# Performance work log

Hardware: AMD Instinct MI355X
Metric: run time of the kernel (lower is better)

The kernel has to match this reference:

```python
import jax, jax.numpy as jnp
import numpy as np

# BoeNet deterministic (greedy) BFS rollout reference.
# Assumptions (source truncated): GrowthPolicyNet ~ Linear(H,1)+sigmoid applied to
# node hidden + DEPTH_EMBED_SCALE * depth_embedding; greedy path expands when
# prob > greedy_threshold. Tree is materialized as a complete binary tree up to
# max_depth with per-node active masks (jit-friendly; honors data-dependent growth
# via masking instead of dynamic shapes). Pooling: mean over active nodes.

V, E, H = 32000, 512, 512
MAX_DEPTH = 3
DEPTH_EMBED_SCALE = 0.01
GREEDY_THRESHOLD = 0.5
PROB_MIN, PROB_MAX = 1e-7, 1.0 - 1e-7
EPS = 1e-8
SIB_SCALE = 1.0 / np.sqrt(H)


def setup_inputs() -> dict:
    key = jax.random.key(0)
    ks = jax.random.split(key, 8)
    B, S = 8, 512
    return {
        "tokens": jax.random.randint(ks[0], (B, S), 0, V),
        "emb": jax.random.normal(ks[1], (V, E), jnp.float32) * 0.02,
        "Wp": jax.random.normal(ks[2], (E, H), jnp.float32) / np.sqrt(E),
        "bp": jnp.zeros((H,), jnp.float32),
        "Wc": jax.random.normal(ks[3], (H, 2 * H), jnp.float32) / np.sqrt(H),
        "bc": jnp.zeros((2 * H,), jnp.float32),
        "Wg": jax.random.normal(ks[4], (H, 1), jnp.float32) / np.sqrt(H),
        "bg": jnp.zeros((1,), jnp.float32),
        "dep": jax.random.normal(ks[5], (MAX_DEPTH + 1, H), jnp.float32) * 0.01,
        "sib": jax.random.normal(ks[6], (2, H), jnp.float32) * 0.02,
        "Wout": jax.random.normal(ks[7], (H, V), jnp.float32) / np.sqrt(H),
        "bout": jnp.zeros((V,), jnp.float32),
    }


def reference(tokens, emb, Wp, bp, Wc, bc, Wg, bg, dep, sib, Wout, bout):
    B, S = tokens.shape
    N = B * S
    # h0: embedding lookup + projection, flattened to positions [N, H]
    h0 = (emb[tokens.reshape(N)] @ Wp + bp)  # [N, H]

    nodes = h0[:, None, :]                    # [N, 1, H] level-0 nodes
    active = jnp.ones((N, 1), h0.dtype)
    agg_sum = h0                              # root always counted
    agg_count = jnp.ones((N,), h0.dtype)

    for d in range(MAX_DEPTH):
        n = nodes.shape[1]
        # growth policy: sigmoid gate on node hidden + scaled depth embedding
        gate_in = nodes + DEPTH_EMBED_SCALE * dep[d]
        prob = jax.nn.sigmoid(jnp.einsum('nkh,ho->nko', gate_in, Wg)[..., 0] + bg[0])
        prob = jnp.clip(prob, PROB_MIN, PROB_MAX)           # [N, n]
        expand = (prob > GREEDY_THRESHOLD).astype(h0.dtype) * active  # [N, n]
        # children: Linear(H, 2H) split into left/right, plus sibling embeddings
        ch = (jnp.einsum('nkh,hj->nkj', nodes, Wc) + bc).reshape(N, 2 * n, H)
        sib_idx = jnp.tile(jnp.arange(2), n)                # [0,1,0,1,...]
        ch = ch + SIB_SCALE * sib[sib_idx]
        ch_active = jnp.repeat(expand, 2, axis=1)           # [N, 2n]
        agg_sum = agg_sum + jnp.einsum('nkh,nk->nh', ch, ch_active)
        agg_count = agg_count + ch_active.sum(axis=1)
        nodes, active = ch, ch_active

    pooled = agg_sum / jnp.maximum(agg_count, EPS)[:, None]  # mean pooling
    logits = pooled @ Wout + bout                            # [N, V]
    return logits.reshape(B, S, V)
```

## Files before the change

### kernel.cpp

```cpp
#include <hip/hip_runtime.h>
#include <cstdint>

#define BM 128
#define BN 128
#define BK 32

typedef __attribute__((ext_vector_type(8))) short short8;
typedef _Float16 half8 __attribute__((ext_vector_type(8)));
typedef __attribute__((ext_vector_type(4))) float floatx4;

union H8 { short8 s; half8 h; };

static constexpr float SIBS   = 0.044194173824159216f;
static constexpr float LS_INV = 1.0f / 2048.0f;

__device__ __forceinline__ unsigned short f2bf(float x){
    union { float f; unsigned u32; } v; v.f = x;
    unsigned r = ((v.u32 >> 16) & 1u) + 0x7fffu;
    return (unsigned short)((v.u32 + r) >> 16);
}
__device__ __forceinline__ void split_f16(float x, unsigned short& h, unsigned short& s){
    _Float16 hh = (_Float16)x;
    _Float16 ss = (_Float16)((x - (float)hh) * 2048.0f);
    union { _Float16 f; unsigned short u; } a, b;
    a.f = hh; b.f = ss;
    h = a.u; s = b.u;
}

#define GLDS(g, l) __builtin_amdgcn_global_load_lds( \
    (const __attribute__((address_space(1))) void*)(g), \
    (__attribute__((address_space(3))) void*)(l), 16, 0, 0)

__global__ void prep_split16_T(const float* __restrict__ src,
                               unsigned short* __restrict__ hiT,
                               unsigned short* __restrict__ lsT,
                               int R, int C)
{
    __shared__ float t[32][33];
    int c0 = blockIdx.x * 32, r0 = blockIdx.y * 32;
    int tx = threadIdx.x & 31, ty = threadIdx.x >> 5;
#pragma unroll
    for (int k = 0; k < 4; k++){
        int r = ty + k*8;
        t[r][tx] = src[(size_t)(r0 + r) * C + c0 + tx];
    }
    __syncthreads();
#pragma unroll
    for (int k = 0; k < 4; k++){
        int r = ty + k*8;
        float x = t[tx][r];
        unsigned short h, s;
        split_f16(x, h, s);
        size_t o = (size_t)(c0 + r) * R + r0 + tx;
        hiT[o] = h; lsT[o] = s;
    }
}

__global__ void prep_bf16_T(const float* __restrict__ src,
                            unsigned short* __restrict__ dstT,
                            int R, int C)
{
    __shared__ float t[32][33];
    int c0 = blockIdx.x * 32, r0 = blockIdx.y * 32;
    int tx = threadIdx.x & 31, ty = threadIdx.x >> 5;
#pragma unroll
    for (int k = 0; k < 4; k++){
        int r = ty + k*8;
        t[r][tx] = src[(size_t)(r0 + r) * C + c0 + tx];
    }
    __syncthreads();
#pragma unroll
    for (int k = 0; k < 4; k++){
        int r = ty + k*8;
        dstT[(size_t)(c0 + r) * R + r0 + tx] = f2bf(t[tx][r]);
    }
}

template<int MODE, int DEPTH>
__global__ __launch_bounds__(256, 2)
void gemm_k(const unsigned short* __restrict__ Abf,
            const float* __restrict__ Af32,
            const unsigned short* __restrict__ BTh,
            const unsigned short* __restrict__ BTl,
            const float* __restrict__ bias,
            const int* __restrict__ tokens,
            const float* __restrict__ emb,
            const float* __restrict__ sib,
            const unsigned char* __restrict__ eflag,
            float* __restrict__ nodes_next,
            float* __restrict__ agg,
            float* __restrict__ f32out,
            float* __restrict__ out,
            int N)
{
    constexpr int K = 512;
    __shared__ __align__(16) unsigned short Ah[BM*BK];
    __shared__ __align__(16) unsigned short Al[BM*BK];
    __shared__ __align__(16) unsigned short Bh[BK*BN];
    __shared__ __align__(16) unsigned short Bl[BK*BN];

    const int tid = threadIdx.x;
    const int w = tid >> 6, l = tid & 63;
    const int wr = w >> 1, wc = w & 1;
    const int row0 = blockIdx.x * BM;
    const int n0   = blockIdx.y * BN;
    const int q = l >> 4, lm = l & 15;

    floatx4 acc[4][4]  = {};
    floatx4 accx[4][4] = {};

    const float* aptr = nullptr;
    const int am = tid & 127, kq0 = tid >> 7;
    if (MODE == 0)      aptr = emb  + (long)tokens[row0 + am] * K;
    else if (MODE == 1) aptr = Af32 + (long)(row0 + am) * K;

    long arow0 = 0, arow1 = 0;
    if (MODE == 2){
        arow0 = (long)(row0 + l) * K;
        arow1 = (long)(row0 + 64 + l) * K;
    }
    const long brow0 = (long)(n0 + l) * K;
    const long brow1 = (long)(n0 + 64 + l) * K;

    for (int k0 = 0; k0 < K; k0 += BK){
        __syncthreads();
        GLDS(BTh + brow0 + k0 + w*8, (char*)Bh + w*2048);
        GLDS(BTh + brow1 + k0 + w*8, (char*)Bh + w*2048 + 1024);
        if (MODE <= 1){
            GLDS(BTl + brow0 + k0 + w*8, (char*)Bl + w*2048);
            GLDS(BTl + brow1 + k0 + w*8, (char*)Bl + w*2048 + 1024);
#pragma unroll
            for (int t = 0; t < 2; t++){
                int kq = kq0 + 2*t;
                const float* src = aptr + k0 + kq*8;
                float xs[8];
                *(floatx4*)&xs[0] = *(const floatx4*)(src);
                *(floatx4*)&xs[4] = *(const floatx4*)(src + 4);
                unsigned short h8[8], l8[8];
#pragma unroll
                for (int e = 0; e < 8; e++) split_f16(xs[e], h8[e], l8[e]);
                int s = kq*128 + am;
                *(short8*)&Ah[s*8] = *(const short8*)h8;
                *(short8*)&Al[s*8] = *(const short8*)l8;
            }
        } else {
            GLDS(Abf + arow0 + k0 + w*8, (char*)Ah + w*2048);
            GLDS(Abf + arow1 + k0 + w*8, (char*)Ah + w*2048 + 1024);
        }
        __syncthreads();

        H8 bh[4], bl[4];
#pragma unroll
        for (int j = 0; j < 4; j++){
            bh[j].s = *(const short8*)&Bh[(q*128 + wc*64 + j*16 + lm)*8];
            if (MODE <= 1)
                bl[j].s = *(const short8*)&Bl[(q*128 + wc*64 + j*16 + lm)*8];
        }
#pragma unroll
        for (int i = 0; i < 4; i++){
            H8 ah; ah.s = *(const short8*)&Ah[(q*128 + wr*64 + i*16 + lm)*8];
            if (MODE <= 1){
                H8 al; al.s = *(const short8*)&Al[(q*128 + wr*64 + i*16 + lm)*8];
#pragma unroll
                for (int j = 0; j < 4; j++)
                    acc[i][j]  = __builtin_amdgcn_mfma_f32_16x16x32_f16(ah.h, bh[j].h, acc[i][j], 0, 0, 0);
#pragma unroll
                for (int j = 0; j < 4; j++)
                    accx[i][j] = __builtin_amdgcn_mfma_f32_16x16x32_f16(ah.h, bl[j].h, accx[i][j], 0, 0, 0);
#pragma unroll
                for (int j = 0; j < 4; j++)
                    accx[i][j] = __builtin_amdgcn_mfma_f32_16x16x32_f16(al.h, bh[j].h, accx[i][j], 0, 0, 0);
            } else {
#pragma unroll
                for (int j = 0; j < 4; j++)
                    acc[i][j] = __builtin_amdgcn_mfma_f32_16x16x32_bf16(ah.s, bh[j].s, acc[i][j], 0, 0, 0);
            }
        }
    }

#pragma unroll
    for (int i = 0; i < 4; i++){
        int rbase = row0 + wr*64 + i*16 + q*4;
        unsigned char fl[4];
        if (MODE == 1){
#pragma unroll
            for (int r = 0; r < 4; r++) fl[r] = eflag[rbase + r];
        }
#pragma unroll
        for (int j = 0; j < 4; j++){
            int col = n0 + wc*64 + j*16 + lm;
            float badd = bias[col];
            int half = 0, h = 0;
            if (MODE == 1){
                half = col >> 9; h = col & 511;
                badd += SIBS * sib[half*512 + h];
            }
#pragma unroll
            for (int r = 0; r < 4; r++){
                int row = rbase + r;
                float v = acc[i][j][r];
                if (MODE <= 1) v += accx[i][j][r] * LS_INV;
                v += badd;
                if (MODE == 0){
                    f32out[(long)row*512 + col] = v;
                    agg[(long)row*512 + col]    = v;
                } else if (MODE == 1){
                    if (DEPTH < 2)
                        nodes_next[((long)(2*row + half))*512 + h] = v;
                    if (fl[r])
                        atomicAdd(&agg[((long)(row >> DEPTH))*512 + h], v);
                } else {
                    out[(long)row*(long)N + col] = v;
                }
            }
        }
    }
}

__global__ void gate_k(const float* __restrict__ nodes,
                       const float* __restrict__ Wg,
                       const float* __restrict__ bg,
                       const float* __restrict__ deprow,
                       const unsigned char* __restrict__ eprev,
                       unsigned char* __restrict__ e,
                       int depth)
{
    int row = blockIdx.x * 4 + (threadIdx.x >> 6);
    int l = threadIdx.x & 63;
    const float* nr = nodes + (long)row * 512;
    float s = 0.f;
#pragma unroll
    for (int t = 0; t < 8; t++){
        int h = t*64 + l;
        s += (nr[h] + 0.01f * deprow[h]) * Wg[h];
    }
#pragma unroll
    for (int off = 32; off > 0; off >>= 1) s += __shfl_down(s, off);
    if (l == 0){
        float x = s + bg[0];
        unsigned char a = (depth == 0) ? (unsigned char)1 : eprev[row >> 1];
        e[row] = (unsigned char)((x > 0.f) && a);
    }
}

__global__ void pool_k(const float* __restrict__ agg,
                       const unsigned char* __restrict__ e0,
                       const unsigned char* __restrict__ e1,
                       const unsigned char* __restrict__ e2,
                       unsigned short* __restrict__ pooled)
{
    int n = blockIdx.x;
    float cnt = 1.f + 2.f * ((float)e0[n] + (float)e1[2*n] + (float)e1[2*n+1]
              + (float)e2[4*n] + (float)e2[4*n+1] + (float)e2[4*n+2] + (float)e2[4*n+3]);
    float inv = 1.f / cnt;
    const float* a = agg + (long)n*512;
    unsigned short* p = pooled + (long)n*512;
    for (int c = threadIdx.x; c < 512; c += 256)
        p[c] = f2bf(a[c] * inv);
}

extern "C" void kernel_launch(void* const* d_in, const int* in_sizes, int n_in,
                              void* d_out, int out_size, void* d_ws, size_t ws_size,
                              hipStream_t stream)
{
    const int*   tokens = (const int*)d_in[0];
    const float* emb    = (const float*)d_in[1];
    const float* Wp     = (const float*)d_in[2];
    const float* bp     = (const float*)d_in[3];
    const float* Wc     = (const float*)d_in[4];
    const float* bc     = (const float*)d_in[5];
    const float* Wg     = (const float*)d_in[6];
    const float* bg     = (const float*)d_in[7];
    const float* dep    = (const float*)d_in[8];
    const float* sib    = (const float*)d_in[9];
    const float* Wout   = (const float*)d_in[10];
    const float* bout   = (const float*)d_in[11];

    if (ws_size < ((size_t)59 << 20)) return;

    char* w = (char*)d_ws;
    auto alloc = [&](size_t bytes)->char*{
        char* p = w; w += (bytes + 255) & ~(size_t)255; return p;
    };
    unsigned short* WpT_h  = (unsigned short*)alloc((size_t)512*512*2);
    unsigned short* WpT_l  = (unsigned short*)alloc((size_t)512*512*2);
    unsigned short* WcT_h  = (unsigned short*)alloc((size_t)1024*512*2);
    unsigned short* WcT_l  = (unsigned short*)alloc((size_t)1024*512*2);
    unsigned short* WoutT  = (unsigned short*)alloc((size_t)32000*512*2);
    float*          nodes0 = (float*)alloc((size_t)4096*512*4);
    float*          agg    = (float*)alloc((size_t)4096*512*4);
    unsigned short* pooled = (unsigned short*)alloc((size_t)4096*512*2);
    unsigned char*  e0     = (unsigned char*)alloc(4096);
    unsigned char*  e1     = (unsigned char*)alloc(8192);
    unsigned char*  e2     = (unsigned char*)alloc(16384);

    float* nodes1 = (float*)d_out;
    float* nodes2 = (float*)((char*)d_out + ((size_t)64 << 20));
    float* out    = (float*)d_out;

    prep_split16_T<<<dim3(512/32,   512/32), 256, 0, stream>>>(Wp,   WpT_h, WpT_l, 512, 512);
    prep_split16_T<<<dim3(1024/32,  512/32), 256, 0, stream>>>(Wc,   WcT_h, WcT_l, 512, 1024);
    prep_bf16_T   <<<dim3(32000/32, 512/32), 256, 0, stream>>>(Wout, WoutT, 512, 32000);

    gemm_k<0,0><<<dim3(32, 4), 256, 0, stream>>>(nullptr, nullptr, WpT_h, WpT_l, bp,
        tokens, emb, nullptr, nullptr, nullptr, agg, nodes0, nullptr, 512);

    gate_k<<<4096/4, 256, 0, stream>>>(nodes0, Wg, bg, dep + 0, nullptr, e0, 0);

    gemm_k<1,0><<<dim3(32, 8), 256, 0, stream>>>(nullptr, nodes0, WcT_h, WcT_l, bc,
        nullptr, nullptr, sib, e0, nodes1, agg, nullptr, nullptr, 1024);

    gate_k<<<8192/4, 256, 0, stream>>>(nodes1, Wg, bg, dep + 512, e0, e1, 1);

    gemm_k<1,1><<<dim3(64, 8), 256, 0, stream>>>(nullptr, nodes1, WcT_h, WcT_l, bc,
        nullptr, nullptr, sib, e1, nodes2, agg, nullptr, nullptr, 1024);

    gate_k<<<16384/4, 256, 0, stream>>>(nodes2, Wg, bg, dep + 1024, e1, e2, 2);

    gemm_k<1,2><<<dim3(128, 8), 256, 0, stream>>>(nullptr, nodes2, WcT_h, WcT_l, bc,
        nullptr, nullptr, sib, e2, nullptr, agg, nullptr, nullptr, 1024);

    pool_k<<<4096, 256, 0, stream>>>(agg, e0, e1, e2, pooled);

    gemm_k<2,0><<<dim3(32, 250), 256, 0, stream>>>(pooled, nullptr, WoutT, nullptr, bout,
        nullptr, nullptr, nullptr, nullptr, nullptr, nullptr, nullptr, out, 32000);
}
```

Measured before the change: 1.051 ms.

## Replace last-level child GEMM with linearity-based masked sum and summed-weight GEMM

Uses the linearity of the child projection: the sum over both children of an expanded node equals the node times (Wc_left+Wc_right) plus the summed biases. The depth-2 child GEMM (the largest one, 16384 rows by 1024 columns) and the atomic aggregation are replaced by a masked-sum kernel and a 4096x512 GEMM against a precomputed summed weight, which also fuses in the mean pooling. Node activations are pre-split into f16 hi/lo planes in the GEMM epilogues so later GEMMs load A directly via global-to-LDS instead of converting in the main loop. This adds an extra pass over the stored node tensors and changes the accumulation order, so floating-point results may differ slightly.

Measured after the change: 1.008 ms. -4.2%, faster.

```diff
diff --git a/kernel.cpp b/kernel.cpp
--- a/kernel.cpp
+++ b/kernel.cpp
@@ -56,6 +56,31 @@
     }
 }
 
+__global__ void prep_wc2_T(const float* __restrict__ Wc,
+                           unsigned short* __restrict__ hiT,
+                           unsigned short* __restrict__ lsT)
+{
+    __shared__ float t[32][33];
+    int c0 = blockIdx.x * 32, r0 = blockIdx.y * 32;
+    int tx = threadIdx.x & 31, ty = threadIdx.x >> 5;
+#pragma unroll
+    for (int k = 0; k < 4; k++){
+        int r = ty + k*8;
+        t[r][tx] = Wc[(size_t)(r0 + r) * 1024 + c0 + tx]
+                 + Wc[(size_t)(r0 + r) * 1024 + 512 + c0 + tx];
+    }
+    __syncthreads();
+#pragma unroll
+    for (int k = 0; k < 4; k++){
+        int r = ty + k*8;
+        float x = t[tx][r];
+        unsigned short h, s;
+        split_f16(x, h, s);
+        size_t o = (size_t)(c0 + r) * 512 + r0 + tx;
+        hiT[o] = h; lsT[o] = s;
+    }
+}
+
 __global__ void prep_bf16_T(const float* __restrict__ src,
                             unsigned short* __restrict__ dstT,
                             int R, int C)
@@ -79,17 +104,22 @@
 template<int MODE, int DEPTH>
 __global__ __launch_bounds__(256, 2)
 void gemm_k(const unsigned short* __restrict__ Abf,
-            const float* __restrict__ Af32,
+            const unsigned short* __restrict__ Agh,
+            const unsigned short* __restrict__ Agl,
             const unsigned short* __restrict__ BTh,
             const unsigned short* __restrict__ BTl,
             const float* __restrict__ bias,
             const int* __restrict__ tokens,
             const float* __restrict__ emb,
             const float* __restrict__ sib,
-            const unsigned char* __restrict__ eflag,
+            const float* __restrict__ mArr,
+            const float* __restrict__ cinv,
+            const float* __restrict__ h0,
             float* __restrict__ nodes_next,
-            float* __restrict__ agg,
+            unsigned short* __restrict__ nxh,
+            unsigned short* __restrict__ nxl,
             float* __restrict__ f32out,
+            unsigned short* __restrict__ pooled,
             float* __restrict__ out,
             int N)
 {
@@ -111,11 +141,10 @@
 
     const float* aptr = nullptr;
     const int am = tid & 127, kq0 = tid >> 7;
-    if (MODE == 0)      aptr = emb  + (long)tokens[row0 + am] * K;
-    else if (MODE == 1) aptr = Af32 + (long)(row0 + am) * K;
+    if (MODE == 0) aptr = emb + (long)tokens[row0 + am] * K;
 
     long arow0 = 0, arow1 = 0;
-    if (MODE == 2){
+    if (MODE != 0){
         arow0 = (long)(row0 + l) * K;
         arow1 = (long)(row0 + 64 + l) * K;
     }
@@ -126,9 +155,19 @@
         __syncthreads();
         GLDS(BTh + brow0 + k0 + w*8, (char*)Bh + w*2048);
         GLDS(BTh + brow1 + k0 + w*8, (char*)Bh + w*2048 + 1024);
-        if (MODE <= 1){
+        if (MODE != 2){
             GLDS(BTl + brow0 + k0 + w*8, (char*)Bl + w*2048);
             GLDS(BTl + brow1 + k0 + w*8, (char*)Bl + w*2048 + 1024);
+        }
+        if (MODE == 1 || MODE == 3){
+            GLDS(Agh + arow0 + k0 + w*8, (char*)Ah + w*2048);
+            GLDS(Agh + arow1 + k0 + w*8, (char*)Ah + w*2048 + 1024);
+            GLDS(Agl + arow0 + k0 + w*8, (char*)Al + w*2048);
+            GLDS(Agl + arow1 + k0 + w*8, (char*)Al + w*2048 + 1024);
+        } else if (MODE == 2){
+            GLDS(Abf + arow0 + k0 + w*8, (char*)Ah + w*2048);
+            GLDS(Abf + arow1 + k0 + w*8, (char*)Ah + w*2048 + 1024);
+        } else {
 #pragma unroll
             for (int t = 0; t < 2; t++){
                 int kq = kq0 + 2*t;
@@ -143,9 +182,6 @@
                 *(short8*)&Ah[s*8] = *(const short8*)h8;
                 *(short8*)&Al[s*8] = *(const short8*)l8;
             }
-        } else {
-            GLDS(Abf + arow0 + k0 + w*8, (char*)Ah + w*2048);
-            GLDS(Abf + arow1 + k0 + w*8, (char*)Ah + w*2048 + 1024);
         }
         __syncthreads();
 
@@ -153,13 +189,13 @@
 #pragma unroll
         for (int j = 0; j < 4; j++){
             bh[j].s = *(const short8*)&Bh[(q*128 + wc*64 + j*16 + lm)*8];
-            if (MODE <= 1)
+            if (MODE != 2)
                 bl[j].s = *(const short8*)&Bl[(q*128 + wc*64 + j*16 + lm)*8];
         }
 #pragma unroll
         for (int i = 0; i < 4; i++){
             H8 ah; ah.s = *(const short8*)&Ah[(q*128 + wr*64 + i*16 + lm)*8];
-            if (MODE <= 1){
+            if (MODE != 2){
                 H8 al; al.s = *(const short8*)&Al[(q*128 + wr*64 + i*16 + lm)*8];
 #pragma unroll
                 for (int j = 0; j < 4; j++)
@@ -181,36 +217,43 @@
 #pragma unroll
     for (int i = 0; i < 4; i++){
         int rbase = row0 + wr*64 + i*16 + q*4;
-        unsigned char fl[4];
-        if (MODE == 1){
-#pragma unroll
-            for (int r = 0; r < 4; r++) fl[r] = eflag[rbase + r];
-        }
 #pragma unroll
         for (int j = 0; j < 4; j++){
             int col = n0 + wc*64 + j*16 + lm;
-            float badd = bias[col];
+            float badd = 0.f, bsum = 0.f;
             int half = 0, h = 0;
+            if (MODE == 0 || MODE == 2) badd = bias[col];
             if (MODE == 1){
                 half = col >> 9; h = col & 511;
-                badd += SIBS * sib[half*512 + h];
+                badd = bias[col] + SIBS * sib[half*512 + h];
             }
+            if (MODE == 3)
+                bsum = bias[col] + bias[512 + col] + SIBS * (sib[col] + sib[512 + col]);
 #pragma unroll
             for (int r = 0; r < 4; r++){
                 int row = rbase + r;
                 float v = acc[i][j][r];
-                if (MODE <= 1) v += accx[i][j][r] * LS_INV;
-                v += badd;
+                if (MODE != 2) v += accx[i][j][r] * LS_INV;
                 if (MODE == 0){
-                    f32out[(long)row*512 + col] = v;
-                    agg[(long)row*512 + col]    = v;
+                    v += badd;
+                    long o = (long)row*512 + col;
+                    f32out[o] = v;
+                    unsigned short hh, ss; split_f16(v, hh, ss);
+                    nxh[o] = hh; nxl[o] = ss;
                 } else if (MODE == 1){
-                    if (DEPTH < 2)
-                        nodes_next[((long)(2*row + half))*512 + h] = v;
-                    if (fl[r])
-                        atomicAdd(&agg[((long)(row >> DEPTH))*512 + h], v);
+                    v += badd;
+                    long o = (long)(2*row + half)*512 + h;
+                    nodes_next[o] = v;
+                    if (DEPTH == 0){
+                        unsigned short hh, ss; split_f16(v, hh, ss);
+                        nxh[o] = hh; nxl[o] = ss;
+                    }
+                } else if (MODE == 3){
+                    long o = (long)row*512 + col;
+                    float outv = (h0[o] + v + mArr[row]*bsum) * cinv[row];
+                    pooled[o] = f2bf(outv);
                 } else {
-                    out[(long)row*(long)N + col] = v;
+                    out[(long)row*(long)N + col] = v + badd;
                 }
             }
         }
@@ -243,20 +286,39 @@
     }
 }
 
-__global__ void pool_k(const float* __restrict__ agg,
+__global__ void msum_k(const float* __restrict__ nodes0,
+                       const float* __restrict__ nodes1,
+                       const float* __restrict__ nodes2,
                        const unsigned char* __restrict__ e0,
                        const unsigned char* __restrict__ e1,
                        const unsigned char* __restrict__ e2,
-                       unsigned short* __restrict__ pooled)
+                       unsigned short* __restrict__ Sh,
+                       unsigned short* __restrict__ Sl,
+                       float* __restrict__ mArr,
+                       float* __restrict__ cinv)
 {
     int n = blockIdx.x;
-    float cnt = 1.f + 2.f * ((float)e0[n] + (float)e1[2*n] + (float)e1[2*n+1]
-              + (float)e2[4*n] + (float)e2[4*n+1] + (float)e2[4*n+2] + (float)e2[4*n+3]);
-    float inv = 1.f / cnt;
-    const float* a = agg + (long)n*512;
-    unsigned short* p = pooled + (long)n*512;
-    for (int c = threadIdx.x; c < 512; c += 256)
-        p[c] = f2bf(a[c] * inv);
+    float a0  = (float)e0[n];
+    float a10 = (float)e1[2*n],   a11 = (float)e1[2*n+1];
+    float a20 = (float)e2[4*n],   a21 = (float)e2[4*n+1];
+    float a22 = (float)e2[4*n+2], a23 = (float)e2[4*n+3];
+    if (threadIdx.x == 0){
+        float m = a0 + a10 + a11 + a20 + a21 + a22 + a23;
+        mArr[n] = m;
+        cinv[n] = 1.f / (1.f + 2.f * m);
+    }
+    const float* p0 = nodes0 + (long)n * 512;
+    const float* p1 = nodes1 + (long)(2*n) * 512;
+    const float* p2 = nodes2 + (long)(4*n) * 512;
+    for (int c = threadIdx.x; c < 512; c += 256){
+        float s = a0 * p0[c]
+                + a10 * p1[c]        + a11 * p1[512 + c]
+                + a20 * p2[c]        + a21 * p2[512 + c]
+                + a22 * p2[1024 + c] + a23 * p2[1536 + c];
+        unsigned short hh, ss; split_f16(s, hh, ss);
+        long o = (long)n * 512 + c;
+        Sh[o] = hh; Sl[o] = ss;
+    }
 }
 
 extern "C" void kernel_launch(void* const* d_in, const int* in_sizes, int n_in,
@@ -276,7 +338,7 @@
     const float* Wout   = (const float*)d_in[10];
     const float* bout   = (const float*)d_in[11];
 
-    if (ws_size < ((size_t)59 << 20)) return;
+    if (ws_size < ((size_t)48 << 20)) return;
 
     char* w = (char*)d_ws;
     auto alloc = [&](size_t bytes)->char*{
@@ -286,42 +348,59 @@
     unsigned short* WpT_l  = (unsigned short*)alloc((size_t)512*512*2);
     unsigned short* WcT_h  = (unsigned short*)alloc((size_t)1024*512*2);
     unsigned short* WcT_l  = (unsigned short*)alloc((size_t)1024*512*2);
+    unsigned short* Wc2T_h = (unsigned short*)alloc((size_t)512*512*2);
+    unsigned short* Wc2T_l = (unsigned short*)alloc((size_t)512*512*2);
     unsigned short* WoutT  = (unsigned short*)alloc((size_t)32000*512*2);
-    float*          nodes0 = (float*)alloc((size_t)4096*512*4);
-    float*          agg    = (float*)alloc((size_t)4096*512*4);
     unsigned short* pooled = (unsigned short*)alloc((size_t)4096*512*2);
     unsigned char*  e0     = (unsigned char*)alloc(4096);
     unsigned char*  e1     = (unsigned char*)alloc(8192);
     unsigned char*  e2     = (unsigned char*)alloc(16384);
 
-    float* nodes1 = (float*)d_out;
-    float* nodes2 = (float*)((char*)d_out + ((size_t)64 << 20));
-    float* out    = (float*)d_out;
-
-    prep_split16_T<<<dim3(512/32,   512/32), 256, 0, stream>>>(Wp,   WpT_h, WpT_l, 512, 512);
-    prep_split16_T<<<dim3(1024/32,  512/32), 256, 0, stream>>>(Wc,   WcT_h, WcT_l, 512, 1024);
-    prep_bf16_T   <<<dim3(32000/32, 512/32), 256, 0, stream>>>(Wout, WoutT, 512, 32000);
-
-    gemm_k<0,0><<<dim3(32, 4), 256, 0, stream>>>(nullptr, nullptr, WpT_h, WpT_l, bp,
-        tokens, emb, nullptr, nullptr, nullptr, agg, nodes0, nullptr, 512);
-
-    gate_k<<<4096/4, 256, 0, stream>>>(nodes0, Wg, bg, dep + 0, nullptr, e0, 0);
-
-    gemm_k<1,0><<<dim3(32, 8), 256, 0, stream>>>(nullptr, nodes0, WcT_h, WcT_l, bc,
-        nullptr, nullptr, sib, e0, nodes1, agg, nullptr, nullptr, 1024);
-
-    gate_k<<<8192/4, 256, 0, stream>>>(nodes1, Wg, bg, dep + 512, e0, e1, 1);
-
-    gemm_k<1,1><<<dim3(64, 8), 256, 0, stream>>>(nullptr, nodes1, WcT_h, WcT_l, bc,
-        nullptr, nullptr, sib, e1, nodes2, agg, nullptr, nullptr, 1024);
-
-    gate_k<<<16384/4, 256, 0, stream>>>(nodes2, Wg, bg, dep + 1024, e1, e2, 2);
-
-    gemm_k<1,2><<<dim3(128, 8), 256, 0, stream>>>(nullptr, nodes2, WcT_h, WcT_l, bc,
-        nullptr, nullptr, sib, e2, nullptr, agg, nullptr, nullptr, 1024);
-
-    pool_k<<<4096, 256, 0, stream>>>(agg, e0, e1, e2, pooled);
-
-    gemm_k<2,0><<<dim3(32, 250), 256, 0, stream>>>(pooled, nullptr, WoutT, nullptr, bout,
-        nullptr, nullptr, nullptr, nullptr, nullptr, nullptr, nullptr, out, 32000);
-}
+    char* ob = (char*)d_out;
+    float*          nodes0 = (float*)(ob + ((size_t) 64 << 20));
+    unsigned short* n0h    = (unsigned short*)(ob + ((size_t) 80 << 20));
+    unsigned short* n0l    = (unsigned short*)(ob + ((size_t) 88 << 20));
+    float*          nodes1 = (float*)(ob + ((size_t) 96 << 20));
+    unsigned short* n1h    = (unsigned short*)(ob + ((size_t)128 << 20));
+    unsigned short* n1l    = (unsigned short*)(ob + ((size_t)144 << 20));
+    float*          nodes2 = (float*)(ob + ((size_t)160 << 20));
+    unsigned short* Sh     = (unsigned short*)(ob + ((size_t)200 << 20));
+    unsigned short* Sl     = (unsigned short*)(ob + ((size_t)208 << 20));
+    float*          mArr   = (float*)(ob + ((size_t)216 << 20));
+    float*          cinvA  = (float*)(ob + ((size_t)217 << 20));
+    float*          out    = (float*)d_out;
+
+    prep_split16_T<<<dim3(16, 16),   256, 0, stream>>>(Wp, WpT_h, WpT_l, 512, 512);
+    prep_split16_T<<<dim3(32, 16),   256, 0, stream>>>(Wc, WcT_h, WcT_l, 512, 1024);
+    prep_wc2_T    <<<dim3(16, 16),   256, 0, stream>>>(Wc, Wc2T_h, Wc2T_l);
+    prep_bf16_T   <<<dim3(1000, 16), 256, 0, stream>>>(Wout, WoutT, 512, 32000);
+
+    gemm_k<0,0><<<dim3(32, 4), 256, 0, stream>>>(nullptr, nullptr, nullptr,
+        WpT_h, WpT_l, bp, tokens, emb, nullptr, nullptr, nullptr, nullptr,
+        nullptr, n0h, n0l, nodes0, nullptr, nullptr, 512);
+
+    gate_k<<<1024, 256, 0, stream>>>(nodes0, Wg, bg, dep + 0, nullptr, e0, 0);
+
+    gemm_k<1,0><<<dim3(32, 8), 256, 0, stream>>>(nullptr, n0h, n0l,
+        WcT_h, WcT_l, bc, nullptr, nullptr, sib, nullptr, nullptr, nullptr,
+        nodes1, n1h, n1l, nullptr, nullptr, nullptr, 1024);
+
+    gate_k<<<2048, 256, 0, stream>>>(nodes1, Wg, bg, dep + 512, e0, e1, 1);
+
+    gemm_k<1,1><<<dim3(64, 8), 256, 0, stream>>>(nullptr, n1h, n1l,
+        WcT_h, WcT_l, bc, nullptr, nullptr, sib, nullptr, nullptr, nullptr,
+        nodes2, nullptr, nullptr, nullptr, nullptr, nullptr, 1024);
+
+    gate_k<<<4096, 256, 0, stream>>>(nodes2, Wg, bg, dep + 1024, e1, e2, 2);
+
+    msum_k<<<4096, 256, 0, stream>>>(nodes0, nodes1, nodes2, e0, e1, e2,
+        Sh, Sl, mArr, cinvA);
+
+    gemm_k<3,0><<<dim3(32, 4), 256, 0, stream>>>(nullptr, Sh, Sl,
+        Wc2T_h, Wc2T_l, bc, nullptr, nullptr, sib, mArr, cinvA, nodes0,
+        nullptr, nullptr, nullptr, nullptr, pooled, nullptr, 512);
+
+    gemm_k<2,0><<<dim3(32, 250), 256, 0, stream>>>(pooled, nullptr, nullptr,
+        WoutT, nullptr, bout, nullptr, nullptr, nullptr, nullptr, nullptr, nullptr,
+        nullptr, nullptr, nullptr, nullptr, nullptr, out, 32000);
+}
```
